# Kernel optimization log

Hardware: AMD Instinct MI355X
Metric: run time of the kernel (lower is better)

The kernel has to match this reference:

```python
import jax, jax.numpy as jnp
import numpy as np

HQ, HKV, HD = 32, 8, 64
ROPE_BASE = 10000.0


def _rope_cos_sin(L):
    # torchtune-style interleaved RoPE cache
    theta = 1.0 / (ROPE_BASE ** (jnp.arange(0, HD, 2, dtype=jnp.float32) / HD))  # [HD/2]
    ang = jnp.arange(L, dtype=jnp.float32)[:, None] * theta[None, :]             # [L, HD/2]
    return jnp.cos(ang)[None, :, None, :], jnp.sin(ang)[None, :, None, :]        # [1,L,1,HD/2]


def _apply_rope(t, cos, sin):
    # t: [B, L, H, HD]; pairs are interleaved along last dim
    x = t.reshape(t.shape[:-1] + (HD // 2, 2))
    x0, x1 = x[..., 0], x[..., 1]
    out = jnp.stack([x0 * cos - x1 * sin, x1 * cos + x0 * sin], axis=-1)
    return out.reshape(t.shape)


def setup_inputs() -> dict:
    key = jax.random.key(0)
    k1, k2, k3 = jax.random.split(key, 3)
    B, L, D = 2, 2048, 2048
    x = jax.random.normal(k1, (B, L, D), dtype=jnp.float32)
    w_qkv = jax.random.normal(k2, ((HQ + 2 * HKV) * HD, D), dtype=jnp.float32) * 0.02
    w_o = jax.random.normal(k3, (D, D), dtype=jnp.float32) * 0.02
    return {"x": x, "w_qkv": w_qkv, "w_o": w_o}


def reference(x, w_qkv, w_o):
    B, L, D = x.shape
    G = HQ // HKV  # q heads per kv head
    qkv = x @ w_qkv.T  # [B, L, (HQ+2*HKV)*HD]
    q = qkv[..., : HQ * HD].reshape(B, L, HQ, HD)
    k = qkv[..., HQ * HD : (HQ + HKV) * HD].reshape(B, L, HKV, HD)
    v = qkv[..., (HQ + HKV) * HD :].reshape(B, L, HKV, HD)

    cos, sin = _rope_cos_sin(L)
    q = _apply_rope(q, cos, sin)
    k = _apply_rope(k, cos, sin)

    # GQA: q head h attends with kv head h // G
    q = q.transpose(0, 2, 1, 3).reshape(B, HKV, G, L, HD)
    k = k.transpose(0, 2, 1, 3)  # [B, HKV, L, HD]
    v = v.transpose(0, 2, 1, 3)

    scale = 1.0 / jnp.sqrt(jnp.float32(HD))
    scores = jnp.einsum('bhgqd,bhkd->bhgqk', q, k) * scale  # [B,HKV,G,L,L]
    causal = jnp.tril(jnp.ones((L, L), dtype=bool))
    scores = jnp.where(causal, scores, jnp.finfo(scores.dtype).min)
    attn = jax.nn.softmax(scores, axis=-1)
    y = jnp.einsum('bhgqk,bhkd->bhgqd', attn, v)            # [B,HKV,G,L,HD]
    y = y.reshape(B, HQ, L, HD).transpose(0, 2, 1, 3).reshape(B, L, D)
    return y @ w_o.T
```

## Files before the change

kernel.cpp:

```cpp
#include <hip/hip_runtime.h>

typedef __attribute__((ext_vector_type(8))) short bf16x8;
typedef __attribute__((ext_vector_type(4))) float f32x4;

__device__ __forceinline__ float bf2f(unsigned short u) {
  unsigned int x = ((unsigned int)u) << 16;
  float f; __builtin_memcpy(&f, &x, 4); return f;
}
__device__ __forceinline__ unsigned short f2bf(float f) {
  unsigned int x; __builtin_memcpy(&x, &f, 4);
  unsigned int lsb = (x >> 16) & 1u;
  x += 0x7fffu + lsb;
  return (unsigned short)(x >> 16);
}
__device__ __forceinline__ unsigned short f2bf_trunc(float f) {
  unsigned int x; __builtin_memcpy(&x, &f, 4);
  return (unsigned short)(x >> 16);
}
__device__ __forceinline__ float exp2_raw(float x) {
  float r;
  asm("v_exp_f32 %0, %1" : "=v"(r) : "v"(x));
  return r;
}
__device__ __forceinline__ void gload16(const unsigned short* g, unsigned short* l) {
  __builtin_amdgcn_global_load_lds(
      (const __attribute__((address_space(1))) unsigned int*)g,
      (__attribute__((address_space(3))) unsigned int*)l, 16, 0, 0);
}

__global__ __launch_bounds__(256) void cvt3(const float* __restrict__ x,
                                            const float* __restrict__ wq,
                                            const float* __restrict__ wo,
                                            unsigned short* __restrict__ xb,
                                            unsigned short* __restrict__ wqb,
                                            unsigned short* __restrict__ wob) {
  const int N0 = 1048576, N1 = 786432, N2 = 524288;
  for (int i = blockIdx.x * 256 + threadIdx.x; i < N0 + N1 + N2;
       i += (int)(gridDim.x * 256)) {
    const float* in; unsigned short* out; int j;
    if (i < N0)            { in = x;  out = xb;  j = i; }
    else if (i < N0 + N1)  { in = wq; out = wqb; j = i - N0; }
    else                   { in = wo; out = wob; j = i - N0 - N1; }
    const float4* p = (const float4*)(in + (size_t)j * 8);
    float4 a = p[0], b = p[1];
    union { bf16x8 v; unsigned short u[8]; } o;
    o.u[0] = f2bf(a.x); o.u[1] = f2bf(a.y); o.u[2] = f2bf(a.z); o.u[3] = f2bf(a.w);
    o.u[4] = f2bf(b.x); o.u[5] = f2bf(b.y); o.u[6] = f2bf(b.z); o.u[7] = f2bf(b.w);
    *(bf16x8*)(out + (size_t)j * 8) = o.v;
  }
}

template <int F32OUT>
__global__ __launch_bounds__(256) void gemm_bt(const unsigned short* __restrict__ A,
                                               const unsigned short* __restrict__ B,
                                               void* __restrict__ Cp, int N) {
  __shared__ unsigned short sA[128 * 64];
  __shared__ unsigned short sB[128 * 64];
  const int t = threadIdx.x;
  const int lane = t & 63, w = t >> 6;
  const int wm = w >> 1, wn = w & 1;
  const int l16 = lane & 15, hi = lane >> 4;
  const int m0 = blockIdx.y * 128, n0 = blockIdx.x * 128;

  f32x4 zero = {0.f, 0.f, 0.f, 0.f};
  f32x4 acc[4][4];
#pragma unroll
  for (int mi = 0; mi < 4; ++mi)
#pragma unroll
    for (int ni = 0; ni < 4; ++ni) acc[mi][ni] = zero;

  const unsigned short* gA = A + (size_t)m0 * 2048;
  const unsigned short* gB = B + (size_t)n0 * 2048;

  for (int k0 = 0; k0 < 2048; k0 += 64) {
    __syncthreads();
#pragma unroll
    for (int i = 0; i < 4; ++i) {
      int c = i * 256 + t;
      int row = c >> 3, cb = c & 7;
      gload16(gA + (size_t)row * 2048 + k0 + ((cb ^ (row & 7)) * 8), &sA[c * 8]);
    }
#pragma unroll
    for (int i = 0; i < 4; ++i) {
      int c = i * 256 + t;
      int row = c >> 3, cb = c & 7;
      gload16(gB + (size_t)row * 2048 + k0 + ((cb ^ (row & 7)) * 8), &sB[c * 8]);
    }
    __syncthreads();
#pragma unroll
    for (int kk = 0; kk < 2; ++kk) {
      bf16x8 af[4], bfr[4];
#pragma unroll
      for (int i = 0; i < 4; ++i) {
        int rowa = wm * 64 + i * 16 + l16;
        af[i]  = *(const bf16x8*)&sA[rowa * 64 + (((kk * 4 + hi) ^ (l16 & 7)) * 8)];
        int rowb = wn * 64 + i * 16 + l16;
        bfr[i] = *(const bf16x8*)&sB[rowb * 64 + (((kk * 4 + hi) ^ (l16 & 7)) * 8)];
      }
#pragma unroll
      for (int mi = 0; mi < 4; ++mi)
#pragma unroll
        for (int ni = 0; ni < 4; ++ni)
          acc[mi][ni] = __builtin_amdgcn_mfma_f32_16x16x32_bf16(af[mi], bfr[ni], acc[mi][ni], 0, 0, 0);
    }
  }

  const int rowb = m0 + wm * 64 + hi * 4;
  const int colb = n0 + wn * 64 + l16;
#pragma unroll
  for (int mi = 0; mi < 4; ++mi)
#pragma unroll
    for (int ni = 0; ni < 4; ++ni)
#pragma unroll
      for (int r = 0; r < 4; ++r) {
        size_t idx = (size_t)(rowb + mi * 16 + r) * N + colb + ni * 16;
        if (F32OUT) ((float*)Cp)[idx] = acc[mi][ni][r];
        else        ((unsigned short*)Cp)[idx] = f2bf(acc[mi][ni][r]);
      }
}

__global__ __launch_bounds__(256) void prep(const unsigned short* __restrict__ qkv,
                                            unsigned short* __restrict__ q,
                                            unsigned short* __restrict__ k,
                                            unsigned short* __restrict__ vt) {
  __shared__ unsigned short sT[64 * 72];
  const int bid = blockIdx.x;
  if (bid < 640) {
    int tid = bid * 256 + threadIdx.x;
    int l = tid & 2047;
    int rest = tid >> 11;
    int b = rest & 1;
    int h = rest >> 1;
    const unsigned short* src = qkv + (size_t)(b * 2048 + l) * 3072 + h * 64;
    union { uint4 v[8]; unsigned short u[64]; } buf;
#pragma unroll
    for (int i = 0; i < 8; ++i) buf.v[i] = ((const uint4*)src)[i];
    const float sc = (h < 32) ? 0.125f * 1.44269504088896f : 1.0f;
#pragma unroll
    for (int j = 0; j < 32; ++j) {
      float fr = exp2f(-(float)j * 0.41524101186092033f);
      float ang = (float)l * fr;
      float sn, cs;
      sincosf(ang, &sn, &cs);
      float x0 = bf2f(buf.u[2 * j]), x1 = bf2f(buf.u[2 * j + 1]);
      float y0 = (x0 * cs - x1 * sn) * sc;
      float y1 = (x1 * cs + x0 * sn) * sc;
      buf.u[2 * j] = f2bf(y0);
      buf.u[2 * j + 1] = f2bf(y1);
    }
    unsigned short* dst = (h < 32) ? (q + ((size_t)(b * 32 + h) * 2048 + l) * 64)
                                   : (k + ((size_t)(b * 8 + h - 32) * 2048 + l) * 64);
#pragma unroll
    for (int i = 0; i < 8; ++i) ((uint4*)dst)[i] = buf.v[i];
  } else {
    const int bid2 = bid - 640;
    const int xb = bid2 & 31, bh = bid2 >> 5;
    const int t = threadIdx.x;
    const int b = bh >> 3, h = bh & 7;
    const int l0 = xb * 64;
    const int c = t & 7, i0 = t >> 3;
#pragma unroll
    for (int pp = 0; pp < 2; ++pp) {
      int i = i0 + pp * 32;
      const unsigned short* src =
          qkv + (size_t)(b * 2048 + l0 + i) * 3072 + 2560 + h * 64 + c * 8;
      union { bf16x8 v; unsigned short u[8]; } x;
      x.v = *(const bf16x8*)src;
#pragma unroll
      for (int e = 0; e < 8; ++e) sT[(c * 8 + e) * 72 + i] = x.u[e];
    }
    __syncthreads();
    const int d = t >> 2, ic = (t & 3) * 16;
    unsigned short* dst = vt + ((size_t)(b * 8 + h) * 64 + d) * 2048 + l0 + ic;
    *(bf16x8*)dst = *(const bf16x8*)&sT[d * 72 + ic];
    *(bf16x8*)(dst + 8) = *(const bf16x8*)&sT[d * 72 + ic + 8];
  }
}

__global__ __launch_bounds__(256) void attn(const unsigned short* __restrict__ Q,
                                            const unsigned short* __restrict__ K,
                                            const unsigned short* __restrict__ VT,
                                            unsigned short* __restrict__ Y) {
  __shared__ unsigned short sK[128 * 64];
  __shared__ unsigned short sV[64 * 128];
  __shared__ unsigned short sP[4][32 * 72];
  const int t = threadIdx.x, lane = t & 63, w = t >> 6;
  const int l16 = lane & 15, hi = lane >> 4;
  const int qb = 15 - (int)blockIdx.y;
  const int bx = blockIdx.x;
  const int head = ((bx & 7) << 3) | (bx >> 3);
  const int b = head >> 5, hq = head & 31, hkv = hq >> 2;
  const unsigned short* kp = K + (size_t)(b * 8 + hkv) * 2048 * 64;
  const unsigned short* vp = VT + (size_t)(b * 8 + hkv) * 64 * 2048;
  unsigned short* sPw = sP[w];
  f32x4 zero = {0.f, 0.f, 0.f, 0.f};
  union { bf16x8 v; unsigned short u[8]; } ones_u;
#pragma unroll
  for (int j = 0; j < 8; ++j) ones_u.u[j] = 0x3F80;
  const bf16x8 ones = ones_u.v;

  const int q0 = qb * 128 + w * 32;
  const unsigned short* qp = Q + ((size_t)(b * 32 + hq) * 2048 + q0) * 64;

  bf16x8 qf[2][2];
#pragma unroll
  for (int mi = 0; mi < 2; ++mi)
#pragma unroll
    for (int ks = 0; ks < 2; ++ks)
      qf[mi][ks] = *(const bf16x8*)(qp + (size_t)(mi * 16 + l16) * 64 + ks * 32 + hi * 8);

  f32x4 o[2][4];
  f32x4 os[2];
#pragma unroll
  for (int mi = 0; mi < 2; ++mi) {
#pragma unroll
    for (int ni = 0; ni < 4; ++ni) o[mi][ni] = zero;
    os[mi] = zero;
  }

  const int nt = qb + 1;
  for (int tt = 0; tt < nt; ++tt) {
    const int c0 = tt * 128;
    __syncthreads();
#pragma unroll
    for (int i = 0; i < 4; ++i) {
      int c = i * 256 + t;
      int row = c >> 3, cb = c & 7;
      gload16(kp + (size_t)(c0 + row) * 64 + ((cb ^ (row & 7)) * 8), &sK[c * 8]);
    }
#pragma unroll
    for (int i = 0; i < 4; ++i) {
      int c = i * 256 + t;
      int d = c >> 4, cb = c & 15;
      gload16(vp + (size_t)d * 2048 + c0 + ((cb ^ (d & 15)) * 8), &sV[c * 8]);
    }
    __syncthreads();

#pragma unroll
    for (int h = 0; h < 2; ++h) {
      const int c0h = c0 + h * 64;
      if (c0h > q0) break;
      f32x4 sc[2][4];
#pragma unroll
      for (int mi = 0; mi < 2; ++mi)
#pragma unroll
        for (int ni = 0; ni < 4; ++ni) sc[mi][ni] = zero;
#pragma unroll
      for (int ni = 0; ni < 4; ++ni) {
        const int krow = h * 64 + ni * 16 + l16;
        bf16x8 k0f = *(const bf16x8*)&sK[krow * 64 + ((hi ^ (l16 & 7)) * 8)];
        bf16x8 k1f = *(const bf16x8*)&sK[krow * 64 + (((4 + hi) ^ (l16 & 7)) * 8)];
#pragma unroll
        for (int mi = 0; mi < 2; ++mi) {
          sc[mi][ni] = __builtin_amdgcn_mfma_f32_16x16x32_bf16(qf[mi][0], k0f, sc[mi][ni], 0, 0, 0);
          sc[mi][ni] = __builtin_amdgcn_mfma_f32_16x16x32_bf16(qf[mi][1], k1f, sc[mi][ni], 0, 0, 0);
        }
      }
      if (c0h + 64 > q0) {
#pragma unroll
        for (int mi = 0; mi < 2; ++mi)
#pragma unroll
          for (int ni = 0; ni < 4; ++ni)
#pragma unroll
            for (int r = 0; r < 4; ++r) {
              int col = c0h + ni * 16 + l16;
              int row = q0 + mi * 16 + hi * 4 + r;
              if (col > row) sc[mi][ni][r] = -1e30f;
            }
      }
#pragma unroll
      for (int mi = 0; mi < 2; ++mi)
#pragma unroll
        for (int ni = 0; ni < 4; ++ni)
#pragma unroll
          for (int r = 0; r < 4; ++r) {
            float p = exp2_raw(sc[mi][ni][r]);
            sPw[(mi * 16 + hi * 4 + r) * 72 + ni * 16 + l16] = f2bf_trunc(p);
          }
#pragma unroll
      for (int ks2 = 0; ks2 < 2; ++ks2) {
        if (c0h + ks2 * 32 > q0) break;
        bf16x8 pa[2];
#pragma unroll
        for (int mi = 0; mi < 2; ++mi) {
          pa[mi] = *(const bf16x8*)&sPw[(mi * 16 + l16) * 72 + ks2 * 32 + hi * 8];
          os[mi] = __builtin_amdgcn_mfma_f32_16x16x32_bf16(pa[mi], ones, os[mi], 0, 0, 0);
        }
#pragma unroll
        for (int ni = 0; ni < 4; ++ni) {
          const int d = ni * 16 + l16;
          bf16x8 vb = *(const bf16x8*)&sV[d * 128 + ((((h * 2 + ks2) * 4 + hi) ^ l16) * 8)];
#pragma unroll
          for (int mi = 0; mi < 2; ++mi)
            o[mi][ni] = __builtin_amdgcn_mfma_f32_16x16x32_bf16(pa[mi], vb, o[mi][ni], 0, 0, 0);
        }
      }
    }
  }
#pragma unroll
  for (int mi = 0; mi < 2; ++mi) {
    float inv[4];
#pragma unroll
    for (int r = 0; r < 4; ++r) inv[r] = 1.f / os[mi][r];
#pragma unroll
    for (int ni = 0; ni < 4; ++ni)
#pragma unroll
      for (int r = 0; r < 4; ++r) {
        int row = q0 + mi * 16 + hi * 4 + r;
        Y[(size_t)(b * 2048 + row) * 2048 + hq * 64 + ni * 16 + l16] =
            f2bf(o[mi][ni][r] * inv[r]);
      }
  }
}

extern "C" void kernel_launch(void* const* d_in, const int* in_sizes, int n_in,
                              void* d_out, int out_size, void* d_ws, size_t ws_size,
                              hipStream_t stream) {
  const float* x    = (const float*)d_in[0];
  const float* wqkv = (const float*)d_in[1];
  const float* wo   = (const float*)d_in[2];
  float* out = (float*)d_out;

  char* ws = (char*)d_ws;
  unsigned short* xb   = (unsigned short*)(ws);
  unsigned short* wqb  = (unsigned short*)(ws + 16777216);
  unsigned short* wob  = (unsigned short*)(ws + 29360128);
  unsigned short* qkvb = (unsigned short*)(ws + 37748736);
  unsigned short* qb   = (unsigned short*)(ws + 62914560);
  unsigned short* kb   = (unsigned short*)(ws + 79691776);
  unsigned short* vtb  = (unsigned short*)(ws + 83886080);
  unsigned short* yb = xb;

  cvt3<<<2048, 256, 0, stream>>>(x, wqkv, wo, xb, wqb, wob);
  gemm_bt<0><<<dim3(3072 / 128, 4096 / 128), 256, 0, stream>>>(xb, wqb, qkvb, 3072);
  prep<<<1152, 256, 0, stream>>>(qkvb, qb, kb, vtb);
  attn<<<dim3(64, 16), 256, 0, stream>>>(qb, kb, vtb, yb);
  gemm_bt<1><<<dim3(2048 / 128, 4096 / 128), 256, 0, stream>>>(yb, wob, out, 2048);
}
```

Before: 196.7 us.

## Add 256x256-tile double-buffered bf16 GEMM for QKV projection

```diff
diff --git a/kernel.cpp b/kernel.cpp
--- a/kernel.cpp
+++ b/kernel.cpp
@@ -27,6 +27,7 @@
       (const __attribute__((address_space(1))) unsigned int*)g,
       (__attribute__((address_space(3))) unsigned int*)l, 16, 0, 0);
 }
+#define RAW_BARRIER() asm volatile("s_barrier" ::: "memory")
 
 __global__ __launch_bounds__(256) void cvt3(const float* __restrict__ x,
                                             const float* __restrict__ wq,
@@ -50,6 +51,130 @@
   }
 }
 
+__global__ __launch_bounds__(512, 2) void gemm256(const unsigned short* __restrict__ A,
+                                                  const unsigned short* __restrict__ B,
+                                                  unsigned short* __restrict__ C, int N) {
+  __shared__ unsigned short sA[2][2][8192];
+  __shared__ unsigned short sB[2][2][8192];
+  const int t = threadIdx.x;
+  const int lane = t & 63, w = t >> 6;
+  const int wm = w >> 2, wn = w & 3;
+  const int l16 = lane & 15, hi = lane >> 4;
+  const int m0 = blockIdx.y * 256, n0 = blockIdx.x * 256;
+  const int sw = (l16 >> 1) & 3;
+
+  f32x4 zero = {0.f, 0.f, 0.f, 0.f};
+  f32x4 acc[8][4];
+#pragma unroll
+  for (int mi = 0; mi < 8; ++mi)
+#pragma unroll
+    for (int ni = 0; ni < 4; ++ni) acc[mi][ni] = zero;
+
+  const unsigned short* gA = A + (size_t)m0 * 2048;
+  const unsigned short* gB = B + (size_t)n0 * 2048;
+
+  auto stage = [&](const unsigned short* g, unsigned short* dst, int k0, int kk) {
+#pragma unroll
+    for (int i = 0; i < 2; ++i) {
+      int c = i * 512 + t;
+      int row = c >> 2, cb = c & 3;
+      gload16(g + (size_t)row * 2048 + k0 + kk * 32 + ((cb ^ ((row >> 1) & 3)) * 8),
+              dst + c * 8);
+    }
+  };
+  auto rdA = [&](int cur, int kk, int mi) -> bf16x8 {
+    int row = wm * 128 + mi * 16 + l16;
+    return *(const bf16x8*)&sA[cur][kk][row * 32 + ((hi ^ sw) * 8)];
+  };
+  auto rdB = [&](int cur, int kk, int ni) -> bf16x8 {
+    int row = wn * 64 + ni * 16 + l16;
+    return *(const bf16x8*)&sB[cur][kk][row * 32 + ((hi ^ sw) * 8)];
+  };
+
+  stage(gA, &sA[0][0][0], 0, 0);
+  stage(gB, &sB[0][0][0], 0, 0);
+  stage(gA, &sA[0][1][0], 0, 1);
+  stage(gB, &sB[0][1][0], 0, 1);
+  asm volatile("s_waitcnt vmcnt(4)" ::: "memory");
+  RAW_BARRIER();
+
+  for (int tt = 0; tt < 32; ++tt) {
+    const int cur = tt & 1, nxt = cur ^ 1;
+    const int k1 = (tt + 1) * 64;
+    const bool pf = (tt < 31);
+    bf16x8 af[4], bfr[4];
+
+#pragma unroll
+    for (int i = 0; i < 4; ++i) af[i] = rdA(cur, 0, i);
+#pragma unroll
+    for (int i = 0; i < 4; ++i) bfr[i] = rdB(cur, 0, i);
+    if (pf) stage(gA, &sA[nxt][0][0], k1, 0);
+    RAW_BARRIER();
+    __builtin_amdgcn_s_setprio(1);
+#pragma unroll
+    for (int mi = 0; mi < 4; ++mi)
+#pragma unroll
+      for (int ni = 0; ni < 4; ++ni)
+        acc[mi][ni] = __builtin_amdgcn_mfma_f32_16x16x32_bf16(af[mi], bfr[ni], acc[mi][ni], 0, 0, 0);
+    __builtin_amdgcn_s_setprio(0);
+    RAW_BARRIER();
+
+#pragma unroll
+    for (int i = 0; i < 4; ++i) af[i] = rdA(cur, 0, 4 + i);
+    if (pf) stage(gB, &sB[nxt][0][0], k1, 0);
+    RAW_BARRIER();
+    __builtin_amdgcn_s_setprio(1);
+#pragma unroll
+    for (int mi = 0; mi < 4; ++mi)
+#pragma unroll
+      for (int ni = 0; ni < 4; ++ni)
+        acc[4 + mi][ni] = __builtin_amdgcn_mfma_f32_16x16x32_bf16(af[mi], bfr[ni], acc[4 + mi][ni], 0, 0, 0);
+    __builtin_amdgcn_s_setprio(0);
+    if (pf) asm volatile("s_waitcnt vmcnt(4)" ::: "memory");
+    else    asm volatile("s_waitcnt vmcnt(0)" ::: "memory");
+    RAW_BARRIER();
+
+#pragma unroll
+    for (int i = 0; i < 4; ++i) af[i] = rdA(cur, 1, i);
+#pragma unroll
+    for (int i = 0; i < 4; ++i) bfr[i] = rdB(cur, 1, i);
+    if (pf) stage(gA, &sA[nxt][1][0], k1, 1);
+    RAW_BARRIER();
+    __builtin_amdgcn_s_setprio(1);
+#pragma unroll
+    for (int mi = 0; mi < 4; ++mi)
+#pragma unroll
+      for (int ni = 0; ni < 4; ++ni)
+        acc[mi][ni] = __builtin_amdgcn_mfma_f32_16x16x32_bf16(af[mi], bfr[ni], acc[mi][ni], 0, 0, 0);
+    __builtin_amdgcn_s_setprio(0);
+    RAW_BARRIER();
+
+#pragma unroll
+    for (int i = 0; i < 4; ++i) af[i] = rdA(cur, 1, 4 + i);
+    if (pf) stage(gB, &sB[nxt][1][0], k1, 1);
+    RAW_BARRIER();
+    __builtin_amdgcn_s_setprio(1);
+#pragma unroll
+    for (int mi = 0; mi < 4; ++mi)
+#pragma unroll
+      for (int ni = 0; ni < 4; ++ni)
+        acc[4 + mi][ni] = __builtin_amdgcn_mfma_f32_16x16x32_bf16(af[mi], bfr[ni], acc[4 + mi][ni], 0, 0, 0);
+    __builtin_amdgcn_s_setprio(0);
+    if (pf) asm volatile("s_waitcnt vmcnt(4)" ::: "memory");
+    RAW_BARRIER();
+  }
+
+  const int rowb = m0 + wm * 128 + hi * 4;
+  const int colb = n0 + wn * 64 + l16;
+#pragma unroll
+  for (int mi = 0; mi < 8; ++mi)
+#pragma unroll
+    for (int ni = 0; ni < 4; ++ni)
+#pragma unroll
+      for (int r = 0; r < 4; ++r)
+        C[(size_t)(rowb + mi * 16 + r) * N + colb + ni * 16] = f2bf(acc[mi][ni][r]);
+}
+
 template <int F32OUT>
 __global__ __launch_bounds__(256) void gemm_bt(const unsigned short* __restrict__ A,
                                                const unsigned short* __restrict__ B,
@@ -332,7 +457,7 @@
   unsigned short* yb = xb;
 
   cvt3<<<2048, 256, 0, stream>>>(x, wqkv, wo, xb, wqb, wob);
-  gemm_bt<0><<<dim3(3072 / 128, 4096 / 128), 256, 0, stream>>>(xb, wqb, qkvb, 3072);
+  gemm256<<<dim3(3072 / 256, 4096 / 256), 512, 0, stream>>>(xb, wqb, qkvb, 3072);
   prep<<<1152, 256, 0, stream>>>(qkvb, qb, kb, vtb);
   attn<<<dim3(64, 16), 256, 0, stream>>>(qb, kb, vtb, yb);
   gemm_bt<1><<<dim3(2048 / 128, 4096 / 128), 256, 0, stream>>>(yb, wob, out, 2048);
```

Result: slower. 210.6 us (+7.1%).

## Fuse RoPE and Q/K head scatter into QKV GEMM epilogue with precomputed trig table

Applied to the files above, without the earlier changes.

```diff
diff --git a/kernel.cpp b/kernel.cpp
--- a/kernel.cpp
+++ b/kernel.cpp
@@ -33,7 +33,8 @@
                                             const float* __restrict__ wo,
                                             unsigned short* __restrict__ xb,
                                             unsigned short* __restrict__ wqb,
-                                            unsigned short* __restrict__ wob) {
+                                            unsigned short* __restrict__ wob,
+                                            float2* __restrict__ trig) {
   const int N0 = 1048576, N1 = 786432, N2 = 524288;
   for (int i = blockIdx.x * 256 + threadIdx.x; i < N0 + N1 + N2;
        i += (int)(gridDim.x * 256)) {
@@ -48,6 +49,102 @@
     o.u[4] = f2bf(b.x); o.u[5] = f2bf(b.y); o.u[6] = f2bf(b.z); o.u[7] = f2bf(b.w);
     *(bf16x8*)(out + (size_t)j * 8) = o.v;
   }
+  for (int e = blockIdx.x * 256 + threadIdx.x; e < 65536;
+       e += (int)(gridDim.x * 256)) {
+    int l = e >> 5, j = e & 31;
+    float fr = exp2f(-(float)j * 0.41524101186092033f);
+    float sn, cs;
+    sincosf((float)l * fr, &sn, &cs);
+    trig[e] = make_float2(cs, sn);
+  }
+}
+
+__global__ __launch_bounds__(256) void gemm_qkv(const unsigned short* __restrict__ A,
+                                                const unsigned short* __restrict__ B,
+                                                unsigned short* __restrict__ qkv,
+                                                unsigned short* __restrict__ q,
+                                                unsigned short* __restrict__ k,
+                                                const float2* __restrict__ trig) {
+  __shared__ unsigned short sA[128 * 64];
+  __shared__ unsigned short sB[128 * 64];
+  const int t = threadIdx.x;
+  const int lane = t & 63, w = t >> 6;
+  const int wm = w >> 1, wn = w & 1;
+  const int l16 = lane & 15, hi = lane >> 4;
+  const int m0 = blockIdx.y * 128, n0 = blockIdx.x * 128;
+
+  f32x4 zero = {0.f, 0.f, 0.f, 0.f};
+  f32x4 acc[4][4];
+#pragma unroll
+  for (int mi = 0; mi < 4; ++mi)
+#pragma unroll
+    for (int ni = 0; ni < 4; ++ni) acc[mi][ni] = zero;
+
+  const unsigned short* gA = A + (size_t)m0 * 2048;
+  const unsigned short* gB = B + (size_t)n0 * 2048;
+
+  for (int k0 = 0; k0 < 2048; k0 += 64) {
+    __syncthreads();
+#pragma unroll
+    for (int i = 0; i < 4; ++i) {
+      int c = i * 256 + t;
+      int row = c >> 3, cb = c & 7;
+      gload16(gA + (size_t)row * 2048 + k0 + ((cb ^ (row & 7)) * 8), &sA[c * 8]);
+    }
+#pragma unroll
+    for (int i = 0; i < 4; ++i) {
+      int c = i * 256 + t;
+      int row = c >> 3, cb = c & 7;
+      gload16(gB + (size_t)row * 2048 + k0 + ((cb ^ (row & 7)) * 8), &sB[c * 8]);
+    }
+    __syncthreads();
+#pragma unroll
+    for (int kk = 0; kk < 2; ++kk) {
+      bf16x8 af[4], bfr[4];
+#pragma unroll
+      for (int i = 0; i < 4; ++i) {
+        int rowa = wm * 64 + i * 16 + l16;
+        af[i]  = *(const bf16x8*)&sA[rowa * 64 + (((kk * 4 + hi) ^ (l16 & 7)) * 8)];
+        int rowb = wn * 64 + i * 16 + l16;
+        bfr[i] = *(const bf16x8*)&sB[rowb * 64 + (((kk * 4 + hi) ^ (l16 & 7)) * 8)];
+      }
+#pragma unroll
+      for (int mi = 0; mi < 4; ++mi)
+#pragma unroll
+        for (int ni = 0; ni < 4; ++ni)
+          acc[mi][ni] = __builtin_amdgcn_mfma_f32_16x16x32_bf16(af[mi], bfr[ni], acc[mi][ni], 0, 0, 0);
+    }
+  }
+
+  const int rowb = m0 + wm * 64 + hi * 4;
+  const int colb = n0 + wn * 64 + l16;
+#pragma unroll
+  for (int mi = 0; mi < 4; ++mi)
+#pragma unroll
+    for (int ni = 0; ni < 4; ++ni) {
+      const int col = colb + ni * 16;
+#pragma unroll
+      for (int r = 0; r < 4; ++r) {
+        const int row = rowb + mi * 16 + r;
+        float v = acc[mi][ni][r];
+        float partner = __shfl_xor(v, 1);
+        const int bb = row >> 11, l = row & 2047;
+        if (col < 2560) {
+          const int j = (col & 63) >> 1;
+          float2 cs = trig[l * 32 + j];
+          float y = (col & 1) ? (v * cs.x + partner * cs.y)
+                              : (v * cs.x - partner * cs.y);
+          if (col < 2048) {
+            y *= 0.18033688011112045f;
+            q[((size_t)(bb * 32 + (col >> 6)) * 2048 + l) * 64 + (col & 63)] = f2bf(y);
+          } else {
+            k[((size_t)(bb * 8 + ((col - 2048) >> 6)) * 2048 + l) * 64 + (col & 63)] = f2bf(y);
+          }
+        } else {
+          qkv[(size_t)(bb * 2048 + l) * 3072 + col] = f2bf(v);
+        }
+      }
+    }
 }
 
 template <int F32OUT>
@@ -119,62 +216,30 @@
       }
 }
 
-__global__ __launch_bounds__(256) void prep(const unsigned short* __restrict__ qkv,
-                                            unsigned short* __restrict__ q,
-                                            unsigned short* __restrict__ k,
-                                            unsigned short* __restrict__ vt) {
+__global__ __launch_bounds__(256) void vtrans(const unsigned short* __restrict__ qkv,
+                                              unsigned short* __restrict__ vt) {
   __shared__ unsigned short sT[64 * 72];
-  const int bid = blockIdx.x;
-  if (bid < 640) {
-    int tid = bid * 256 + threadIdx.x;
-    int l = tid & 2047;
-    int rest = tid >> 11;
-    int b = rest & 1;
-    int h = rest >> 1;
-    const unsigned short* src = qkv + (size_t)(b * 2048 + l) * 3072 + h * 64;
-    union { uint4 v[8]; unsigned short u[64]; } buf;
-#pragma unroll
-    for (int i = 0; i < 8; ++i) buf.v[i] = ((const uint4*)src)[i];
-    const float sc = (h < 32) ? 0.125f * 1.44269504088896f : 1.0f;
-#pragma unroll
-    for (int j = 0; j < 32; ++j) {
-      float fr = exp2f(-(float)j * 0.41524101186092033f);
-      float ang = (float)l * fr;
-      float sn, cs;
-      sincosf(ang, &sn, &cs);
-      float x0 = bf2f(buf.u[2 * j]), x1 = bf2f(buf.u[2 * j + 1]);
-      float y0 = (x0 * cs - x1 * sn) * sc;
-      float y1 = (x1 * cs + x0 * sn) * sc;
-      buf.u[2 * j] = f2bf(y0);
-      buf.u[2 * j + 1] = f2bf(y1);
-    }
-    unsigned short* dst = (h < 32) ? (q + ((size_t)(b * 32 + h) * 2048 + l) * 64)
-                                   : (k + ((size_t)(b * 8 + h - 32) * 2048 + l) * 64);
-#pragma unroll
-    for (int i = 0; i < 8; ++i) ((uint4*)dst)[i] = buf.v[i];
-  } else {
-    const int bid2 = bid - 640;
-    const int xb = bid2 & 31, bh = bid2 >> 5;
-    const int t = threadIdx.x;
-    const int b = bh >> 3, h = bh & 7;
-    const int l0 = xb * 64;
-    const int c = t & 7, i0 = t >> 3;
-#pragma unroll
-    for (int pp = 0; pp < 2; ++pp) {
-      int i = i0 + pp * 32;
-      const unsigned short* src =
-          qkv + (size_t)(b * 2048 + l0 + i) * 3072 + 2560 + h * 64 + c * 8;
-      union { bf16x8 v; unsigned short u[8]; } x;
-      x.v = *(const bf16x8*)src;
-#pragma unroll
-      for (int e = 0; e < 8; ++e) sT[(c * 8 + e) * 72 + i] = x.u[e];
-    }
-    __syncthreads();
-    const int d = t >> 2, ic = (t & 3) * 16;
-    unsigned short* dst = vt + ((size_t)(b * 8 + h) * 64 + d) * 2048 + l0 + ic;
-    *(bf16x8*)dst = *(const bf16x8*)&sT[d * 72 + ic];
-    *(bf16x8*)(dst + 8) = *(const bf16x8*)&sT[d * 72 + ic + 8];
-  }
+  const int bid2 = blockIdx.x;
+  const int xb = bid2 & 31, bh = bid2 >> 5;
+  const int t = threadIdx.x;
+  const int b = bh >> 3, h = bh & 7;
+  const int l0 = xb * 64;
+  const int c = t & 7, i0 = t >> 3;
+#pragma unroll
+  for (int pp = 0; pp < 2; ++pp) {
+    int i = i0 + pp * 32;
+    const unsigned short* src =
+        qkv + (size_t)(b * 2048 + l0 + i) * 3072 + 2560 + h * 64 + c * 8;
+    union { bf16x8 v; unsigned short u[8]; } x;
+    x.v = *(const bf16x8*)src;
+#pragma unroll
+    for (int e = 0; e < 8; ++e) sT[(c * 8 + e) * 72 + i] = x.u[e];
+  }
+  __syncthreads();
+  const int d = t >> 2, ic = (t & 3) * 16;
+  unsigned short* dst = vt + ((size_t)(b * 8 + h) * 64 + d) * 2048 + l0 + ic;
+  *(bf16x8*)dst = *(const bf16x8*)&sT[d * 72 + ic];
+  *(bf16x8*)(dst + 8) = *(const bf16x8*)&sT[d * 72 + ic + 8];
 }
 
 __global__ __launch_bounds__(256) void attn(const unsigned short* __restrict__ Q,
@@ -330,10 +395,11 @@
   unsigned short* kb   = (unsigned short*)(ws + 79691776);
   unsigned short* vtb  = (unsigned short*)(ws + 83886080);
   unsigned short* yb = xb;
-
-  cvt3<<<2048, 256, 0, stream>>>(x, wqkv, wo, xb, wqb, wob);
-  gemm_bt<0><<<dim3(3072 / 128, 4096 / 128), 256, 0, stream>>>(xb, wqb, qkvb, 3072);
-  prep<<<1152, 256, 0, stream>>>(qkvb, qb, kb, vtb);
+  float2* trig = (float2*)((char*)d_out + 33554432 - 524288);
+
+  cvt3<<<2048, 256, 0, stream>>>(x, wqkv, wo, xb, wqb, wob, trig);
+  gemm_qkv<<<dim3(3072 / 128, 4096 / 128), 256, 0, stream>>>(xb, wqb, qkvb, qb, kb, trig);
+  vtrans<<<512, 256, 0, stream>>>(qkvb, vtb);
   attn<<<dim3(64, 16), 256, 0, stream>>>(qb, kb, vtb, yb);
   gemm_bt<1><<<dim3(2048 / 128, 4096 / 128), 256, 0, stream>>>(yb, wob, out, 2048);
 }
```

Result: slower. 227.7 us (+15.8%).
